# Performance work log

Measured on AMD Instinct MI355X. Metric: run time of the kernel, lower is better.

The kernel has to match this reference:

```python
import jax, jax.numpy as jnp
import numpy as np

D_EMBD = 1024
N_HEADS = 16
D_HEAD = D_EMBD // N_HEADS
BS, T = 2, 2048


def setup_inputs() -> dict:
    key = jax.random.key(0)
    ks = jax.random.split(key, 5)
    s1 = 1.0 / np.sqrt(D_EMBD)
    x = jax.random.normal(ks[0], (BS, T, D_EMBD), dtype=jnp.float32)
    # dense1: Linear(d_embd, 3*d_embd); stored as [in, out] matmul matrix
    W1 = jax.random.uniform(ks[1], (D_EMBD, 3 * D_EMBD), jnp.float32, -s1, s1)
    b1 = jax.random.uniform(ks[2], (3 * D_EMBD,), jnp.float32, -s1, s1)
    # dense2: Linear(d_embd, d_embd)
    W2 = jax.random.uniform(ks[3], (D_EMBD, D_EMBD), jnp.float32, -s1, s1)
    b2 = jax.random.uniform(ks[4], (D_EMBD,), jnp.float32, -s1, s1)
    return {"x": x, "W1": W1, "b1": b1, "W2": W2, "b2": b2}


def reference(x, W1, b1, W2, b2):
    bs, t, d = x.shape
    kqv = x @ W1 + b1                               # [b, t, 3d]
    # torch.chunk order in source: k, q, v
    k, q, v = jnp.split(kqv, 3, axis=-1)
    def heads(z):  # [b, t, (h d)] -> [b, h, t, d]
        return z.reshape(bs, t, N_HEADS, D_HEAD).transpose(0, 2, 1, 3)
    k, q, v = heads(k), heads(q), heads(v)
    scale = 1.0 / np.sqrt(D_HEAD).astype(np.float32)
    attn = jnp.einsum('bhtd,bhsd->bhts', q, k) * scale   # [b, h, t, t]
    causal = jnp.tril(jnp.ones((t, t), dtype=bool))
    attn = jnp.where(causal, attn, -jnp.inf)
    attn = jax.nn.softmax(attn, axis=-1)
    out = jnp.einsum('bhts,bhsd->bhtd', attn, v)         # [b, h, t, d]
    out = out.transpose(0, 2, 1, 3).reshape(bs, t, d)    # [b, t, (h d)]
    return out @ W2 + b2
```

## Files before the change

### kernel.cpp

```cpp
#include <hip/hip_runtime.h>

typedef unsigned short ushort_t;
typedef short bf16x8 __attribute__((ext_vector_type(8)));
typedef short bf16x4 __attribute__((ext_vector_type(4)));
typedef float f32x4 __attribute__((ext_vector_type(4)));

__device__ __forceinline__ unsigned f2bf(float f) {
    union { float f; unsigned u; } c; c.f = f;
    unsigned u = c.u;
    u += 0x7FFFu + ((u >> 16) & 1u);
    return u >> 16;
}

__device__ __forceinline__ float bf2f(unsigned lo16) {
    union { unsigned u; float f; } c; c.u = lo16 << 16; return c.f;
}

__device__ __forceinline__ unsigned pack_trunc(float a, float b) {
    union { float f; unsigned u; } ca, cb; ca.f = a; cb.f = b;
    return (ca.u >> 16) | (cb.u & 0xFFFF0000u);
}

__device__ __forceinline__ void async16(const ushort_t* g, ushort_t* l) {
    __builtin_amdgcn_global_load_lds(
        (const __attribute__((address_space(1))) unsigned int*)g,
        (__attribute__((address_space(3))) unsigned int*)l, 16, 0, 0);
}

__global__ __launch_bounds__(256) void prep_kernel(
    const float* __restrict__ x, const float* __restrict__ W1, const float* __restrict__ W2,
    ushort_t* __restrict__ xb, ushort_t* __restrict__ w1t, ushort_t* __restrict__ w2t) {
    __shared__ float tile[64][65];
    const int tid = threadIdx.x;
    const int bid = blockIdx.x;
    if (bid < 2048) {
        const int i = (bid * 256 + tid) * 8;
        const float4 a = *(const float4*)(x + i);
        const float4 b = *(const float4*)(x + i + 4);
        uint4 pk;
        pk.x = f2bf(a.x) | (f2bf(a.y) << 16);
        pk.y = f2bf(a.z) | (f2bf(a.w) << 16);
        pk.z = f2bf(b.x) | (f2bf(b.y) << 16);
        pk.w = f2bf(b.z) | (f2bf(b.w) << 16);
        *(uint4*)(xb + i) = pk;
        return;
    }
    const float* src; ushort_t* dst; int R, C, r0, c0;
    if (bid < 2816) {
        const int t = bid - 2048;
        src = W1; dst = w1t; R = 1024; C = 3072;
        c0 = (t % 48) * 64; r0 = (t / 48) * 64;
    } else {
        const int t = bid - 2816;
        src = W2; dst = w2t; R = 1024; C = 1024;
        c0 = (t & 15) * 64; r0 = (t >> 4) * 64;
    }
    const int rr = tid >> 4, cc = (tid & 15) * 4;
#pragma unroll
    for (int i = 0; i < 4; ++i) {
        const float4 v = *(const float4*)(src + (size_t)(r0 + rr + 16 * i) * C + c0 + cc);
        tile[rr + 16 * i][cc]     = v.x;
        tile[rr + 16 * i][cc + 1] = v.y;
        tile[rr + 16 * i][cc + 2] = v.z;
        tile[rr + 16 * i][cc + 3] = v.w;
    }
    __syncthreads();
#pragma unroll
    for (int i = 0; i < 4; ++i) {
        const int orow = rr + 16 * i;
        uint2 pk;
        pk.x = f2bf(tile[cc][orow])     | (f2bf(tile[cc + 1][orow]) << 16);
        pk.y = f2bf(tile[cc + 2][orow]) | (f2bf(tile[cc + 3][orow]) << 16);
        *(uint2*)(dst + (size_t)(c0 + orow) * R + r0 + cc) = pk;
    }
}

__device__ __forceinline__ void gemm_core_128(const ushort_t* __restrict__ A,
                                              const ushort_t* __restrict__ B,
                                              int m0, int n0,
                                              ushort_t* As, ushort_t* Bs,
                                              f32x4 acc[4][4], int tid) {
    const int w = tid >> 6, lane = tid & 63, quad = lane >> 4, l16 = lane & 15;
    const int wrow = (w >> 1) * 64, wcol = (w & 1) * 64;
    const ushort_t* Ab = A + (size_t)m0 * 1024;
    const ushort_t* Bb = B + (size_t)n0 * 1024;
    for (int kt = 0; kt < 32; ++kt) {
        const int k0 = kt * 32;
#pragma unroll
        for (int c = 0; c < 2; ++c) {
            const int e = c * 2048 + tid * 8;
            const int row = e >> 5, col = e & 31;
            async16(Ab + (size_t)row * 1024 + k0 + col, As + e);
            async16(Bb + (size_t)row * 1024 + k0 + col, Bs + e);
        }
        __syncthreads();
        bf16x8 af[4], bfr[4];
#pragma unroll
        for (int i = 0; i < 4; ++i) {
            af[i]  = *(const bf16x8*)(As + (wrow + i * 16 + l16) * 32 + quad * 8);
            bfr[i] = *(const bf16x8*)(Bs + (wcol + i * 16 + l16) * 32 + quad * 8);
        }
#pragma unroll
        for (int mi = 0; mi < 4; ++mi)
#pragma unroll
            for (int ni = 0; ni < 4; ++ni)
                acc[mi][ni] = __builtin_amdgcn_mfma_f32_16x16x32_bf16(
                    af[mi], bfr[ni], acc[mi][ni], 0, 0, 0);
        __syncthreads();
    }
}

__global__ __launch_bounds__(256) void gemm_qkv_kernel(
    const ushort_t* __restrict__ xb, const ushort_t* __restrict__ w1t,
    const float* __restrict__ b1,
    ushort_t* __restrict__ kb, ushort_t* __restrict__ qb, ushort_t* __restrict__ vb) {
    __shared__ __attribute__((aligned(16))) ushort_t As[128 * 32];
    __shared__ __attribute__((aligned(16))) ushort_t Bs[128 * 32];
    const int tid = threadIdx.x;
    const int id = blockIdx.x;
    const int g = id >> 3;
    const int n0 = (g >> 2) * 128;
    const int m0 = ((id & 7) + 8 * (g & 3)) * 128;
    f32x4 acc[4][4];
    const f32x4 z4 = {0.f, 0.f, 0.f, 0.f};
#pragma unroll
    for (int i = 0; i < 4; ++i)
#pragma unroll
        for (int j = 0; j < 4; ++j) acc[i][j] = z4;
    gemm_core_128(xb, w1t, m0, n0, As, Bs, acc, tid);

    const int w = tid >> 6, lane = tid & 63, quad = lane >> 4, l16 = lane & 15;
    const int wrow = (w >> 1) * 64, wcol = (w & 1) * 64;
    const int chunk = n0 >> 10;
#pragma unroll
    for (int mi = 0; mi < 4; ++mi) {
#pragma unroll
        for (int ni = 0; ni < 4; ++ni) {
            const int cg = n0 + wcol + ni * 16 + l16;
            const float bias = b1[cg];
            const int hc = cg & 1023;
            const int h = hc >> 6, d = hc & 63;
#pragma unroll
            for (int r = 0; r < 4; ++r) {
                const int rg = m0 + wrow + mi * 16 + quad * 4 + r;
                const int bb = rg >> 11, tt = rg & 2047;
                const int bh = bb * 16 + h;
                const float v = acc[mi][ni][r] + bias;
                if (chunk == 0)
                    kb[((size_t)bh * 2048 + tt) * 64 + d] = (ushort_t)f2bf(v);
                else if (chunk == 1)
                    qb[((size_t)bh * 2048 + tt) * 64 + d] = (ushort_t)f2bf(v * 0.1803368801f);
                else
                    vb[((size_t)bh * 64 + d) * 2048 + tt] = (ushort_t)f2bf(v);
            }
        }
    }
}

__device__ __constant__ int4 ATTN_SCHED[24] = {
    {15,  0, 16, 14}, {15, 16, 16, 15}, { 7,  0, 16, -1},
    {14,  0, 15, 12}, {14, 15, 15, 13},
    {13,  0, 14, 10}, {13, 14, 14, 11}, { 6,  0, 14, -1},
    {12,  0, 13,  8}, {12, 13, 13,  9},
    {11,  0, 12,  6}, {11, 12, 12,  7}, { 5,  0, 12, -1},
    {10,  0, 11,  4}, {10, 11, 11,  5},
    { 9,  0, 10,  2}, { 9, 10, 10,  3}, { 4,  0, 10, -1},
    { 8,  0,  9,  0}, { 8,  9,  9,  1},
    { 3,  0,  8, -1}, { 2,  0,  6, -1}, { 1,  0,  4, -1}, { 0,  0,  2, -1}
};

__global__ __launch_bounds__(256) void attn_kernel(
    const ushort_t* __restrict__ qb, const ushort_t* __restrict__ kb,
    const ushort_t* __restrict__ vb,
    ushort_t* __restrict__ Opart, float* __restrict__ lpart,
    ushort_t* __restrict__ aout) {
    __shared__ __attribute__((aligned(16))) ushort_t Ks[2][64][72];
    __shared__ __attribute__((aligned(16))) ushort_t Vs[2][64][72];

    const int tid = threadIdx.x;
    const int w = tid >> 6, lane = tid & 63, quad = lane >> 4, l16 = lane & 15;
    const int bh = blockIdx.x;
    const int4 sc = ATTN_SCHED[blockIdx.y];
    const int qtile = sc.x, k0 = sc.y, kcnt = sc.z, slot_ofs = sc.w;
    const int q0 = qtile * 128;
    const int q0w = q0 + w * 32;
    const int kend = k0 + kcnt;
    const float NEG_INF = -__builtin_inff();

    const ushort_t* Q = qb + (size_t)bh * (2048 * 64);
    const ushort_t* K = kb + (size_t)bh * (2048 * 64);
    const ushort_t* V = vb + (size_t)bh * (64 * 2048);

    bf16x8 aq[2][2];
#pragma unroll
    for (int u = 0; u < 2; ++u)
#pragma unroll
        for (int kh = 0; kh < 2; ++kh)
            aq[u][kh] = *(const bf16x8*)(Q + (size_t)(q0w + u * 16 + l16) * 64 + kh * 32 + quad * 8);

    const int srow = tid >> 2, scol = (tid & 3) * 16;

    uint4 kr0, kr1, vr0, vr1;
    {
        const uint4* kp = (const uint4*)(K + (size_t)(k0 * 64 + srow) * 64 + scol);
        kr0 = kp[0]; kr1 = kp[1];
        const uint4* vp = (const uint4*)(V + (size_t)srow * 2048 + k0 * 64 + scol);
        vr0 = vp[0]; vr1 = vp[1];
    }

    float l_i[2] = {0.f, 0.f};
    f32x4 o[2][4];
    const f32x4 z4 = {0.f, 0.f, 0.f, 0.f};
#pragma unroll
    for (int u = 0; u < 2; ++u)
#pragma unroll
        for (int d = 0; d < 4; ++d) o[u][d] = z4;

    for (int kt = k0; kt < kend; ++kt) {
        const int cur = kt & 1;
        *(uint4*)&Ks[cur][srow][scol]     = kr0;
        *(uint4*)&Ks[cur][srow][scol + 8] = kr1;
        *(uint4*)&Vs[cur][srow][scol]     = vr0;
        *(uint4*)&Vs[cur][srow][scol + 8] = vr1;
        __syncthreads();
        if (kt + 1 < kend) {
            const uint4* kp = (const uint4*)(K + (size_t)((kt + 1) * 64 + srow) * 64 + scol);
            kr0 = kp[0]; kr1 = kp[1];
            const uint4* vp = (const uint4*)(V + (size_t)srow * 2048 + (kt + 1) * 64 + scol);
            vr0 = vp[0]; vr1 = vp[1];
        }
        if (kt * 64 >= q0w + 32) continue;

        bf16x8 af[4][2];
#pragma unroll
        for (int ni = 0; ni < 4; ++ni)
#pragma unroll
            for (int kh = 0; kh < 2; ++kh)
                af[ni][kh] = *(const bf16x8*)&Ks[cur][ni * 16 + l16][kh * 32 + quad * 8];
        f32x4 st[2][4];
#pragma unroll
        for (int u = 0; u < 2; ++u)
#pragma unroll
            for (int ni = 0; ni < 4; ++ni) {
                f32x4 acc = z4;
                acc = __builtin_amdgcn_mfma_f32_16x16x32_bf16(af[ni][0], aq[u][0], acc, 0, 0, 0);
                acc = __builtin_amdgcn_mfma_f32_16x16x32_bf16(af[ni][1], aq[u][1], acc, 0, 0, 0);
                st[u][ni] = acc;
            }
        if (kt >= 2 * qtile) {
#pragma unroll
            for (int u = 0; u < 2; ++u)
#pragma unroll
                for (int ni = 0; ni < 4; ++ni)
#pragma unroll
                    for (int r = 0; r < 4; ++r) {
                        const int s = kt * 64 + ni * 16 + quad * 4 + r;
                        const int q = q0w + u * 16 + l16;
                        if (s > q) st[u][ni][r] = NEG_INF;
                    }
        }
        bf16x4 ph[2][4];
#pragma unroll
        for (int u = 0; u < 2; ++u) {
            float p[4][4], rs = 0.f;
#pragma unroll
            for (int ni = 0; ni < 4; ++ni)
#pragma unroll
                for (int r = 0; r < 4; ++r) {
                    p[ni][r] = __builtin_amdgcn_exp2f(st[u][ni][r]);
                    rs += p[ni][r];
                }
            l_i[u] += rs;
#pragma unroll
            for (int ni = 0; ni < 4; ++ni) {
                union { bf16x4 v; uint2 uu; } pk;
                pk.uu.x = pack_trunc(p[ni][0], p[ni][1]);
                pk.uu.y = pack_trunc(p[ni][2], p[ni][3]);
                ph[u][ni] = pk.v;
            }
        }
#pragma unroll
        for (int ni = 0; ni < 4; ++ni)
#pragma unroll
            for (int dt = 0; dt < 4; ++dt) {
                const bf16x4 av = *(const bf16x4*)&Vs[cur][dt * 16 + l16][ni * 16 + quad * 4];
                o[0][dt] = __builtin_amdgcn_mfma_f32_16x16x16bf16_1k(av, ph[0][ni], o[0][dt], 0, 0, 0);
                o[1][dt] = __builtin_amdgcn_mfma_f32_16x16x16bf16_1k(av, ph[1][ni], o[1][dt], 0, 0, 0);
            }
    }
    if (slot_ofs < 0) {
        const int b = bh >> 4, h = bh & 15;
#pragma unroll
        for (int u = 0; u < 2; ++u) {
            float l = l_i[u];
            l += __shfl_xor(l, 16);
            l += __shfl_xor(l, 32);
            const float inv = 1.0f / l;
            const int q = q0w + u * 16 + l16;
#pragma unroll
            for (int dt = 0; dt < 4; ++dt) {
                uint2 pk;
                pk.x = f2bf(o[u][dt][0] * inv) | (f2bf(o[u][dt][1] * inv) << 16);
                pk.y = f2bf(o[u][dt][2] * inv) | (f2bf(o[u][dt][3] * inv) << 16);
                *(uint2*)&aout[(size_t)(b * 2048 + q) * 1024 + h * 64 + dt * 16 + quad * 4] = pk;
            }
        }
    } else {
        const int slot = bh * 16 + slot_ofs;
#pragma unroll
        for (int u = 0; u < 2; ++u) {
            float l = l_i[u];
            l += __shfl_xor(l, 16);
            l += __shfl_xor(l, 32);
            const int row = w * 32 + u * 16 + l16;
            if (quad == 0) lpart[slot * 128 + row] = l;
#pragma unroll
            for (int dt = 0; dt < 4; ++dt) {
                uint2 pk;
                pk.x = f2bf(o[u][dt][0]) | (f2bf(o[u][dt][1]) << 16);
                pk.y = f2bf(o[u][dt][2]) | (f2bf(o[u][dt][3]) << 16);
                *(uint2*)&Opart[(size_t)slot * 8192 + row * 64 + dt * 16 + quad * 4] = pk;
            }
        }
    }
}

__global__ __launch_bounds__(256) void merge_kernel(
    const ushort_t* __restrict__ Opart, const float* __restrict__ lpart,
    ushort_t* __restrict__ aout) {
    __shared__ float inv[128];
    const int bh = blockIdx.x, qtile = 8 + blockIdx.y;
    const int s0 = bh * 16 + (qtile - 8) * 2;
    const int t = threadIdx.x;
    if (t < 128)
        inv[t] = 1.0f / (lpart[s0 * 128 + t] + lpart[(s0 + 1) * 128 + t]);
    __syncthreads();
    const int b = bh >> 4, h = bh & 15;
#pragma unroll
    for (int i = 0; i < 8; ++i) {
        const int e = i * 1024 + t * 4;
        const int row = e >> 6, d = e & 63;
        const uint2 a = *(const uint2*)&Opart[(size_t)s0 * 8192 + e];
        const uint2 bb = *(const uint2*)&Opart[(size_t)(s0 + 1) * 8192 + e];
        const float v0 = bf2f(a.x & 0xFFFFu) + bf2f(bb.x & 0xFFFFu);
        const float v1 = bf2f(a.x >> 16)     + bf2f(bb.x >> 16);
        const float v2 = bf2f(a.y & 0xFFFFu) + bf2f(bb.y & 0xFFFFu);
        const float v3 = bf2f(a.y >> 16)     + bf2f(bb.y >> 16);
        const float iv = inv[row];
        uint2 opk;
        opk.x = f2bf(v0 * iv) | (f2bf(v1 * iv) << 16);
        opk.y = f2bf(v2 * iv) | (f2bf(v3 * iv) << 16);
        *(uint2*)&aout[(size_t)(b * 2048 + qtile * 128 + row) * 1024 + h * 64 + d] = opk;
    }
}

__global__ __launch_bounds__(256) void gemm_out_kernel(
    const ushort_t* __restrict__ ab, const ushort_t* __restrict__ w2t,
    const float* __restrict__ b2, float* __restrict__ out) {
    __shared__ __attribute__((aligned(16))) ushort_t As[128 * 32];
    __shared__ __attribute__((aligned(16))) ushort_t Bs[64 * 32];
    const int tid = threadIdx.x;
    const int w = tid >> 6, lane = tid & 63, quad = lane >> 4, l16 = lane & 15;
    const int id = blockIdx.x;
    const int g = id >> 3;
    const int n0 = (g >> 2) * 64;
    const int m0 = ((id & 7) + 8 * (g & 3)) * 128;
    f32x4 acc[2][4];
    const f32x4 z4 = {0.f, 0.f, 0.f, 0.f};
#pragma unroll
    for (int i = 0; i < 2; ++i)
#pragma unroll
        for (int j = 0; j < 4; ++j) acc[i][j] = z4;
    const ushort_t* Ab = ab + (size_t)m0 * 1024;
    const ushort_t* Bb = w2t + (size_t)n0 * 1024;
    for (int kt = 0; kt < 32; ++kt) {
        const int k0 = kt * 32;
        {
            const int e = tid * 8;
            async16(Ab + (size_t)(e >> 5) * 1024 + k0 + (e & 31), As + e);
            const int e2 = 2048 + e;
            async16(Ab + (size_t)(e2 >> 5) * 1024 + k0 + (e2 & 31), As + e2);
            async16(Bb + (size_t)(e >> 5) * 1024 + k0 + (e & 31), Bs + e);
        }
        __syncthreads();
        bf16x8 af[2], bfr[4];
#pragma unroll
        for (int mi = 0; mi < 2; ++mi)
            af[mi] = *(const bf16x8*)(As + (w * 32 + mi * 16 + l16) * 32 + quad * 8);
#pragma unroll
        for (int ni = 0; ni < 4; ++ni)
            bfr[ni] = *(const bf16x8*)(Bs + (ni * 16 + l16) * 32 + quad * 8);
#pragma unroll
        for (int mi = 0; mi < 2; ++mi)
#pragma unroll
            for (int ni = 0; ni < 4; ++ni)
                acc[mi][ni] = __builtin_amdgcn_mfma_f32_16x16x32_bf16(
                    af[mi], bfr[ni], acc[mi][ni], 0, 0, 0);
        __syncthreads();
    }
#pragma unroll
    for (int mi = 0; mi < 2; ++mi) {
#pragma unroll
        for (int ni = 0; ni < 4; ++ni) {
            const int cg = n0 + ni * 16 + l16;
            const float bias = b2[cg];
#pragma unroll
            for (int r = 0; r < 4; ++r) {
                const int rg = m0 + w * 32 + mi * 16 + quad * 4 + r;
                out[(size_t)rg * 1024 + cg] = acc[mi][ni][r] + bias;
            }
        }
    }
}

extern "C" void kernel_launch(void* const* d_in, const int* in_sizes, int n_in,
                              void* d_out, int out_size, void* d_ws, size_t ws_size,
                              hipStream_t stream) {
    const float* x  = (const float*)d_in[0];
    const float* W1 = (const float*)d_in[1];
    const float* b1 = (const float*)d_in[2];
    const float* W2 = (const float*)d_in[3];
    const float* b2 = (const float*)d_in[4];
    float* out = (float*)d_out;

    char* ws = (char*)d_ws;
    const size_t MB = 1024 * 1024;
    ushort_t* xb  = (ushort_t*)(ws);
    ushort_t* w1t = (ushort_t*)(ws + 8 * MB);
    ushort_t* w2t = (ushort_t*)(ws + 14 * MB);
    ushort_t* kb  = (ushort_t*)(ws + 16 * MB);
    ushort_t* qb  = (ushort_t*)(ws + 24 * MB);
    ushort_t* vb  = (ushort_t*)(ws + 32 * MB);
    ushort_t* ao  = (ushort_t*)(ws + 40 * MB);
    ushort_t* Opart = (ushort_t*)(ws);
    float*    lpart = (float*)(ws + 13 * MB);

    prep_kernel<<<3072, 256, 0, stream>>>(x, W1, W2, xb, w1t, w2t);
    gemm_qkv_kernel<<<768, 256, 0, stream>>>(xb, w1t, b1, kb, qb, vb);
    attn_kernel<<<dim3(32, 24), 256, 0, stream>>>(qb, kb, vb, Opart, lpart, ao);
    merge_kernel<<<dim3(32, 8), 256, 0, stream>>>(Opart, lpart, ao);
    gemm_out_kernel<<<512, 256, 0, stream>>>(ao, w2t, b2, out);
}
```

Before: 176.5 us.

## Fuse split-KV attention merge into output projection GEMM A-tile load

Removes the separate merge kernel. For query tiles 8-15 of each batch, the output GEMM now builds its A tile by reading the two partial attention outputs and row sums, normalizing them and writing the bf16 result straight into LDS. This saves a kernel launch and the write and re-read of the merged activation. In exchange, each of the 16 N-blocks repeats the merge for its M tile, and those blocks lose the async LDS load path.

```diff
diff --git a/kernel.cpp b/kernel.cpp
--- a/kernel.cpp
+++ b/kernel.cpp
@@ -325,37 +325,29 @@
     }
 }
 
-__global__ __launch_bounds__(256) void merge_kernel(
-    const ushort_t* __restrict__ Opart, const float* __restrict__ lpart,
-    ushort_t* __restrict__ aout) {
-    __shared__ float inv[128];
-    const int bh = blockIdx.x, qtile = 8 + blockIdx.y;
-    const int s0 = bh * 16 + (qtile - 8) * 2;
-    const int t = threadIdx.x;
-    if (t < 128)
-        inv[t] = 1.0f / (lpart[s0 * 128 + t] + lpart[(s0 + 1) * 128 + t]);
-    __syncthreads();
-    const int b = bh >> 4, h = bh & 15;
-#pragma unroll
-    for (int i = 0; i < 8; ++i) {
-        const int e = i * 1024 + t * 4;
-        const int row = e >> 6, d = e & 63;
-        const uint2 a = *(const uint2*)&Opart[(size_t)s0 * 8192 + e];
-        const uint2 bb = *(const uint2*)&Opart[(size_t)(s0 + 1) * 8192 + e];
-        const float v0 = bf2f(a.x & 0xFFFFu) + bf2f(bb.x & 0xFFFFu);
-        const float v1 = bf2f(a.x >> 16)     + bf2f(bb.x >> 16);
-        const float v2 = bf2f(a.y & 0xFFFFu) + bf2f(bb.y & 0xFFFFu);
-        const float v3 = bf2f(a.y >> 16)     + bf2f(bb.y >> 16);
-        const float iv = inv[row];
-        uint2 opk;
-        opk.x = f2bf(v0 * iv) | (f2bf(v1 * iv) << 16);
-        opk.y = f2bf(v2 * iv) | (f2bf(v3 * iv) << 16);
-        *(uint2*)&aout[(size_t)(b * 2048 + qtile * 128 + row) * 1024 + h * 64 + d] = opk;
-    }
+__device__ __forceinline__ void merge16(const ushort_t* __restrict__ Opart,
+                                        const float* __restrict__ lpart,
+                                        int slot, int row, int dcol, ushort_t* dst) {
+    const uint4 o1 = *(const uint4*)(Opart + (size_t)slot * 8192 + row * 64 + dcol);
+    const uint4 o2 = *(const uint4*)(Opart + (size_t)(slot + 1) * 8192 + row * 64 + dcol);
+    const float iv = __builtin_amdgcn_rcpf(
+        lpart[slot * 128 + row] + lpart[(slot + 1) * 128 + row]);
+    const unsigned* p1 = (const unsigned*)&o1;
+    const unsigned* p2 = (const unsigned*)&o2;
+    uint4 res;
+    unsigned* pr = (unsigned*)&res;
+#pragma unroll
+    for (int i = 0; i < 4; ++i) {
+        const float lo = (bf2f(p1[i] & 0xFFFFu) + bf2f(p2[i] & 0xFFFFu)) * iv;
+        const float hi = (bf2f(p1[i] >> 16) + bf2f(p2[i] >> 16)) * iv;
+        pr[i] = f2bf(lo) | (f2bf(hi) << 16);
+    }
+    *(uint4*)dst = res;
 }
 
 __global__ __launch_bounds__(256) void gemm_out_kernel(
     const ushort_t* __restrict__ ab, const ushort_t* __restrict__ w2t,
+    const ushort_t* __restrict__ Opart, const float* __restrict__ lpart,
     const float* __restrict__ b2, float* __restrict__ out) {
     __shared__ __attribute__((aligned(16))) ushort_t As[128 * 32];
     __shared__ __attribute__((aligned(16))) ushort_t Bs[64 * 32];
@@ -364,7 +356,10 @@
     const int id = blockIdx.x;
     const int g = id >> 3;
     const int n0 = (g >> 2) * 64;
-    const int m0 = ((id & 7) + 8 * (g & 3)) * 128;
+    const int mt = (id & 7) + 8 * (g & 3);
+    const int m0 = mt * 128;
+    const int b = mt >> 4, qtile = mt & 15;
+    const bool merged = qtile >= 8;
     f32x4 acc[2][4];
     const f32x4 z4 = {0.f, 0.f, 0.f, 0.f};
 #pragma unroll
@@ -373,15 +368,20 @@
         for (int j = 0; j < 4; ++j) acc[i][j] = z4;
     const ushort_t* Ab = ab + (size_t)m0 * 1024;
     const ushort_t* Bb = w2t + (size_t)n0 * 1024;
+    const int e0 = tid * 8, e1 = 2048 + tid * 8;
+    const int r0 = e0 >> 5, c0 = e0 & 31, r1 = e1 >> 5, c1 = e1 & 31;
     for (int kt = 0; kt < 32; ++kt) {
         const int k0 = kt * 32;
-        {
-            const int e = tid * 8;
-            async16(Ab + (size_t)(e >> 5) * 1024 + k0 + (e & 31), As + e);
-            const int e2 = 2048 + e;
-            async16(Ab + (size_t)(e2 >> 5) * 1024 + k0 + (e2 & 31), As + e2);
-            async16(Bb + (size_t)(e >> 5) * 1024 + k0 + (e & 31), Bs + e);
-        }
+        if (!merged) {
+            async16(Ab + (size_t)r0 * 1024 + k0 + c0, As + e0);
+            async16(Ab + (size_t)r1 * 1024 + k0 + c1, As + e1);
+        } else {
+            const int h = kt >> 1, d0 = (kt & 1) * 32;
+            const int slot = (b * 16 + h) * 16 + (qtile - 8) * 2;
+            merge16(Opart, lpart, slot, r0, d0 + c0, As + e0);
+            merge16(Opart, lpart, slot, r1, d0 + c1, As + e1);
+        }
+        async16(Bb + (size_t)r0 * 1024 + k0 + c0, Bs + e0);
         __syncthreads();
         bf16x8 af[2], bfr[4];
 #pragma unroll
@@ -438,6 +438,5 @@
     prep_kernel<<<3072, 256, 0, stream>>>(x, W1, W2, xb, w1t, w2t);
     gemm_qkv_kernel<<<768, 256, 0, stream>>>(xb, w1t, b1, kb, qb, vb);
     attn_kernel<<<dim3(32, 24), 256, 0, stream>>>(qb, kb, vb, Opart, lpart, ao);
-    merge_kernel<<<dim3(32, 8), 256, 0, stream>>>(Opart, lpart, ao);
-    gemm_out_kernel<<<512, 256, 0, stream>>>(ao, w2t, b2, out);
-}
+    gemm_out_kernel<<<512, 256, 0, stream>>>(ao, w2t, Opart, lpart, b2, out);
+}
```

After: 192.1 us. +8.8%, slower.

## Fuse split-K attention merge into attention kernel via last-arriver atomic flags

Applied to the files above, without the earlier changes.

Drops the separate merge kernel. Each split-KV attention block writes its partial output, then bumps an atomic counter, and the second block to finish combines its register accumulators with the other block's stored partial and writes the final normalized output. The flags are zeroed inside the QKV GEMM kernel. This removes one kernel launch and a re-read of one partial, at the cost of thread fences, an atomic, and extra tail work in some attention blocks.

```diff
diff --git a/kernel.cpp b/kernel.cpp
--- a/kernel.cpp
+++ b/kernel.cpp
@@ -113,11 +113,13 @@
 __global__ __launch_bounds__(256) void gemm_qkv_kernel(
     const ushort_t* __restrict__ xb, const ushort_t* __restrict__ w1t,
     const float* __restrict__ b1,
-    ushort_t* __restrict__ kb, ushort_t* __restrict__ qb, ushort_t* __restrict__ vb) {
+    ushort_t* __restrict__ kb, ushort_t* __restrict__ qb, ushort_t* __restrict__ vb,
+    int* __restrict__ flags) {
     __shared__ __attribute__((aligned(16))) ushort_t As[128 * 32];
     __shared__ __attribute__((aligned(16))) ushort_t Bs[128 * 32];
     const int tid = threadIdx.x;
     const int id = blockIdx.x;
+    if (id == 0) flags[tid] = 0;
     const int g = id >> 3;
     const int n0 = (g >> 2) * 128;
     const int m0 = ((id & 7) + 8 * (g & 3)) * 128;
@@ -173,9 +175,10 @@
     const ushort_t* __restrict__ qb, const ushort_t* __restrict__ kb,
     const ushort_t* __restrict__ vb,
     ushort_t* __restrict__ Opart, float* __restrict__ lpart,
-    ushort_t* __restrict__ aout) {
+    int* __restrict__ flags, ushort_t* __restrict__ aout) {
     __shared__ __attribute__((aligned(16))) ushort_t Ks[2][64][72];
     __shared__ __attribute__((aligned(16))) ushort_t Vs[2][64][72];
+    __shared__ int last_flag;
 
     const int tid = threadIdx.x;
     const int w = tid >> 6, lane = tid & 63, quad = lane >> 4, l16 = lane & 15;
@@ -288,8 +291,8 @@
                 o[1][dt] = __builtin_amdgcn_mfma_f32_16x16x16bf16_1k(av, ph[1][ni], o[1][dt], 0, 0, 0);
             }
     }
+    const int b = bh >> 4, h = bh & 15;
     if (slot_ofs < 0) {
-        const int b = bh >> 4, h = bh & 15;
 #pragma unroll
         for (int u = 0; u < 2; ++u) {
             float l = l_i[u];
@@ -307,11 +310,13 @@
         }
     } else {
         const int slot = bh * 16 + slot_ofs;
+        float lred[2];
 #pragma unroll
         for (int u = 0; u < 2; ++u) {
             float l = l_i[u];
             l += __shfl_xor(l, 16);
             l += __shfl_xor(l, 32);
+            lred[u] = l;
             const int row = w * 32 + u * 16 + l16;
             if (quad == 0) lpart[slot * 128 + row] = l;
 #pragma unroll
@@ -322,35 +327,31 @@
                 *(uint2*)&Opart[(size_t)slot * 8192 + row * 64 + dt * 16 + quad * 4] = pk;
             }
         }
-    }
-}
-
-__global__ __launch_bounds__(256) void merge_kernel(
-    const ushort_t* __restrict__ Opart, const float* __restrict__ lpart,
-    ushort_t* __restrict__ aout) {
-    __shared__ float inv[128];
-    const int bh = blockIdx.x, qtile = 8 + blockIdx.y;
-    const int s0 = bh * 16 + (qtile - 8) * 2;
-    const int t = threadIdx.x;
-    if (t < 128)
-        inv[t] = 1.0f / (lpart[s0 * 128 + t] + lpart[(s0 + 1) * 128 + t]);
-    __syncthreads();
-    const int b = bh >> 4, h = bh & 15;
-#pragma unroll
-    for (int i = 0; i < 8; ++i) {
-        const int e = i * 1024 + t * 4;
-        const int row = e >> 6, d = e & 63;
-        const uint2 a = *(const uint2*)&Opart[(size_t)s0 * 8192 + e];
-        const uint2 bb = *(const uint2*)&Opart[(size_t)(s0 + 1) * 8192 + e];
-        const float v0 = bf2f(a.x & 0xFFFFu) + bf2f(bb.x & 0xFFFFu);
-        const float v1 = bf2f(a.x >> 16)     + bf2f(bb.x >> 16);
-        const float v2 = bf2f(a.y & 0xFFFFu) + bf2f(bb.y & 0xFFFFu);
-        const float v3 = bf2f(a.y >> 16)     + bf2f(bb.y >> 16);
-        const float iv = inv[row];
-        uint2 opk;
-        opk.x = f2bf(v0 * iv) | (f2bf(v1 * iv) << 16);
-        opk.y = f2bf(v2 * iv) | (f2bf(v3 * iv) << 16);
-        *(uint2*)&aout[(size_t)(b * 2048 + qtile * 128 + row) * 1024 + h * 64 + d] = opk;
+        __threadfence();
+        __syncthreads();
+        if (tid == 0)
+            last_flag = (atomicAdd(&flags[bh * 8 + (qtile - 8)], 1) == 1);
+        __syncthreads();
+        if (last_flag) {
+            __threadfence();
+            const int oslot = slot ^ 1;
+#pragma unroll
+            for (int u = 0; u < 2; ++u) {
+                const int row = w * 32 + u * 16 + l16;
+                const float inv = 1.0f / (lred[u] + lpart[oslot * 128 + row]);
+                const int q = q0w + u * 16 + l16;
+#pragma unroll
+                for (int dt = 0; dt < 4; ++dt) {
+                    const uint2 op = *(const uint2*)&Opart[(size_t)oslot * 8192 + row * 64 + dt * 16 + quad * 4];
+                    uint2 pk;
+                    pk.x = f2bf((o[u][dt][0] + bf2f(op.x & 0xFFFFu)) * inv)
+                         | (f2bf((o[u][dt][1] + bf2f(op.x >> 16)) * inv) << 16);
+                    pk.y = f2bf((o[u][dt][2] + bf2f(op.y & 0xFFFFu)) * inv)
+                         | (f2bf((o[u][dt][3] + bf2f(op.y >> 16)) * inv) << 16);
+                    *(uint2*)&aout[(size_t)(b * 2048 + q) * 1024 + h * 64 + dt * 16 + quad * 4] = pk;
+                }
+            }
+        }
     }
 }
 
@@ -434,10 +435,10 @@
     ushort_t* ao  = (ushort_t*)(ws + 40 * MB);
     ushort_t* Opart = (ushort_t*)(ws);
     float*    lpart = (float*)(ws + 13 * MB);
+    int*      flags = (int*)(ws + 48 * MB);
 
     prep_kernel<<<3072, 256, 0, stream>>>(x, W1, W2, xb, w1t, w2t);
-    gemm_qkv_kernel<<<768, 256, 0, stream>>>(xb, w1t, b1, kb, qb, vb);
-    attn_kernel<<<dim3(32, 24), 256, 0, stream>>>(qb, kb, vb, Opart, lpart, ao);
-    merge_kernel<<<dim3(32, 8), 256, 0, stream>>>(Opart, lpart, ao);
+    gemm_qkv_kernel<<<768, 256, 0, stream>>>(xb, w1t, b1, kb, qb, vb, flags);
+    attn_kernel<<<dim3(32, 24), 256, 0, stream>>>(qb, kb, vb, Opart, lpart, flags, ao);
     gemm_out_kernel<<<512, 256, 0, stream>>>(ao, w2t, b2, out);
 }
```

Result: slower. 271.6 us (+53.9%).
